# Performance work log

Measured on AMD Instinct MI355X. Metric: run time of the kernel, lower is better.

## Reference

```python
import jax, jax.numpy as jnp
import numpy as np

B, S, F, H = 512, 128, 128, 512
TIME_SCALE = 72.0
N_SUB = 8        # fixed RK45 substeps per interval (replaces adaptive dopri5 stepping)
MIN_DT = 1e-4    # torch code skips ODE solve if mean dt <= min_dt
LN_EPS = 1e-5


def setup_inputs() -> dict:
    key = jax.random.key(0)
    ks = jax.random.split(key, 12)
    time_points = jnp.sort(jax.random.uniform(ks[0], (B, S)) * TIME_SCALE, axis=1)
    values = jax.random.normal(ks[1], (B, S, F))
    s1 = 1.0 / np.sqrt(H)
    s2 = 1.0 / np.sqrt(2 * H)
    sg = 1.0 / np.sqrt(H)
    # ODEFunc: Linear(H,2H) -> tanh -> Linear(2H,H); weights stored (in,out)
    w1 = jax.random.uniform(ks[2], (H, 2 * H), minval=-s1, maxval=s1)
    b1 = jax.random.uniform(ks[3], (2 * H,), minval=-s1, maxval=s1)
    w2 = jax.random.uniform(ks[4], (2 * H, H), minval=-s2, maxval=s2)
    b2 = jax.random.uniform(ks[5], (H,), minval=-s2, maxval=s2)
    # GRUCell(F+1, H): torch layout w_ih (3H, F+1), w_hh (3H, H)
    w_ih = jax.random.uniform(ks[6], (3 * H, F + 1), minval=-sg, maxval=sg)
    w_hh = jax.random.uniform(ks[7], (3 * H, H), minval=-sg, maxval=sg)
    b_ih = jax.random.uniform(ks[8], (3 * H,), minval=-sg, maxval=sg)
    b_hh = jax.random.uniform(ks[9], (3 * H,), minval=-sg, maxval=sg)
    gamma = jnp.ones((H,))
    beta = jnp.zeros((H,))
    return {"time_points": time_points, "values": values,
            "w1": w1, "b1": b1, "w2": w2, "b2": b2,
            "w_ih": w_ih, "w_hh": w_hh, "b_ih": b_ih, "b_hh": b_hh,
            "gamma": gamma, "beta": beta}


def reference(time_points, values, w1, b1, w2, b2, w_ih, w_hh, b_ih, b_hh, gamma, beta):
    def ode_f(h):  # autonomous dynamics: 2-layer tanh MLP
        return jnp.tanh(h @ w1 + b1) @ w2 + b2

    def rk45(h, dt):  # Dormand-Prince 5th-order step (fixed step of size dt)
        k1 = ode_f(h)
        k2 = ode_f(h + dt * (1.0 / 5.0) * k1)
        k3 = ode_f(h + dt * (3.0 / 40.0 * k1 + 9.0 / 40.0 * k2))
        k4 = ode_f(h + dt * (44.0 / 45.0 * k1 - 56.0 / 15.0 * k2 + 32.0 / 9.0 * k3))
        k5 = ode_f(h + dt * (19372.0 / 6561.0 * k1 - 25360.0 / 2187.0 * k2
                             + 64448.0 / 6561.0 * k3 - 212.0 / 729.0 * k4))
        k6 = ode_f(h + dt * (9017.0 / 3168.0 * k1 - 355.0 / 33.0 * k2
                             + 46732.0 / 5247.0 * k3 + 49.0 / 176.0 * k4
                             - 5103.0 / 18656.0 * k5))
        return h + dt * (35.0 / 384.0 * k1 + 500.0 / 1113.0 * k3 + 125.0 / 192.0 * k4
                         - 2187.0 / 6784.0 * k5 + 11.0 / 84.0 * k6)

    batch, seq, _ = values.shape
    hdim = w_hh.shape[1]
    t_scaled_mean = (time_points / TIME_SCALE).mean(axis=0)  # (S,)
    dt_mean = jnp.concatenate([jnp.zeros((1,)), jnp.diff(t_scaled_mean)])  # (S,)
    dt_raw = jnp.concatenate([jnp.zeros((batch, 1)), jnp.diff(time_points, axis=1)], axis=1)  # (B,S)

    def step(h, inp):
        x, dti, dtm = inp  # x:(B,F), dti:(B,1), dtm: scalar
        dt_eff = jnp.where(dtm > MIN_DT, dtm, 0.0)
        sub = dt_eff / N_SUB
        h = jax.lax.fori_loop(0, N_SUB, lambda i, hh: rk45(hh, sub), h)
        x_aug = jnp.concatenate([x, dti], axis=-1)  # (B, F+1)
        gi = x_aug @ w_ih.T + b_ih
        gh = h @ w_hh.T + b_hh
        r = jax.nn.sigmoid(gi[:, :hdim] + gh[:, :hdim])
        z = jax.nn.sigmoid(gi[:, hdim:2 * hdim] + gh[:, hdim:2 * hdim])
        n = jnp.tanh(gi[:, 2 * hdim:] + r * gh[:, 2 * hdim:])
        h_new = (1.0 - z) * n + z * h
        return h_new, h_new

    h0 = jnp.zeros((batch, hdim), dtype=values.dtype)
    xs = (values.transpose(1, 0, 2), dt_raw.T[..., None], dt_mean)
    _, hs = jax.lax.scan(step, h0, xs)  # (S,B,H)
    rnn_out = hs.transpose(1, 0, 2)  # (B,S,H)
    mu = rnn_out.mean(axis=-1, keepdims=True)
    var = rnn_out.var(axis=-1, keepdims=True)
    return (rnn_out - mu) / jnp.sqrt(var + LN_EPS) * gamma + beta
```

## Files before the change

kernel.cpp:

```cpp
#include <hip/hip_runtime.h>
#include <cstdint>
#include <cstddef>

#define Bsz 512
#define Ssz 128
#define Fsz 128
#define Hsz 512
#define NTWO 1024

typedef __attribute__((ext_vector_type(8))) short short8;
typedef __attribute__((ext_vector_type(4))) float f32x4;
typedef unsigned int u32;
typedef unsigned short u16;

__device__ __forceinline__ float b2f(u16 u){
  union { u32 i; float f; } v; v.i = ((u32)u) << 16; return v.f;
}
__device__ __forceinline__ u16 f2b(float f){
  union { float f; u32 i; } v; v.f = f;
  u32 x = v.i;
  return (u16)((x + 0x7fffu + ((x >> 16) & 1u)) >> 16);
}
template<int AUX>
__device__ __forceinline__ void g2l16(const void* g, void* l){
  __builtin_amdgcn_global_load_lds((const __attribute__((address_space(1))) u32*)g,
                                   (__attribute__((address_space(3))) u32*)l, 16, 0, AUX);
}
__device__ __forceinline__ void st_devf(float* p, float v){
  __hip_atomic_store(p, v, __ATOMIC_RELAXED, __HIP_MEMORY_SCOPE_AGENT);
}
__device__ __forceinline__ void stg16_sc(void* p, short8 v){
  asm volatile("global_store_dwordx4 %0, %1, off sc0 sc1" :: "v"(p), "v"(v) : "memory");
}
__device__ __forceinline__ short8 ldg16(const void* p){
  short8 r;
  asm volatile("global_load_dwordx4 %0, %1, off" : "=v"(r) : "v"(p) : "memory");
  return r;
}
__device__ __forceinline__ float ftanh(float x){
  float a = fabsf(x);
  float e = __expf(-2.f*a);
  float t = __fdividef(1.f - e, 1.f + e);
  return copysignf(t, x);
}
__device__ __forceinline__ void vwait(int n){
  switch(n){
    case 0: asm volatile("s_waitcnt vmcnt(0)" ::: "memory"); break;
    case 1: asm volatile("s_waitcnt vmcnt(1)" ::: "memory"); break;
    case 2: asm volatile("s_waitcnt vmcnt(2)" ::: "memory"); break;
    case 4: asm volatile("s_waitcnt vmcnt(4)" ::: "memory"); break;
    default: break;
  }
}

#define RB1 0.09114583333333333f
#define RB3 0.4492362982929021f
#define RB4 0.6510416666666666f
#define RB5 (-0.3223921568627451f)
#define RB6 0.13095238095238096f
#define MFMA16 __builtin_amdgcn_mfma_f32_16x16x32_bf16


__global__ void zero_k(float* h, u16* h2, u32* bar){
  int i = blockIdx.x*256 + threadIdx.x;
  if (i < Bsz*Hsz) h[i] = 0.f;
  h2[i] = 0;
  if (i < 512) bar[i] = 0u;
}

__global__ void tsm_k(const float* tp, float* tsm){
  int s = blockIdx.x, tid = threadIdx.x;
  __shared__ float red[8];
  float v = tp[(size_t)tid*Ssz + s] + tp[(size_t)(tid + 256)*Ssz + s];
  int wave = tid >> 6, lane = tid & 63;
  for (int o = 32; o; o >>= 1) v += __shfl_down(v, o);
  if (!lane) red[wave] = v;
  __syncthreads();
  if (!tid) tsm[s] = (red[0] + red[1] + red[2] + red[3]) * (1.f/(512.f*72.f));
}

__global__ void sub_k(const float* tsm, float* subs){
  int i = threadIdx.x;
  if (i < Ssz){
    float dtm = (i == 0) ? 0.f : (tsm[i] - tsm[i-1]);
    float de = (dtm > 1e-4f) ? dtm : 0.f;
    subs[i] = de * 0.125f;
  }
}

__global__ void dti_k(const float* tp, float* dti){
  int i = blockIdx.x*256 + threadIdx.x;
  int ss = i & 127;
  dti[i] = ss ? (tp[i] - tp[i-1]) : 0.f;
}

__global__ void tr1_k(const float* w1, u16* lin, u16* swz){
  int i = blockIdx.x*256 + threadIdx.x;
  int n = i >> 9, k = i & 511;
  u16 v = f2b(w1[(size_t)k*NTWO + n]);
  lin[i] = v;
  swz[(size_t)n*512 + (k ^ ((n&7)<<3))] = v;
}

__global__ void cvt_k(const float* src, u16* dst, int n){
  int i = blockIdx.x*256 + threadIdx.x;
  if (i < n) dst[i] = f2b(src[i]);
}

__global__ void w2t_k(const float* w2, u16* dst){
  int i = blockIdx.x*256 + threadIdx.x;
  int n = i >> 10, k = i & 1023;
  dst[(size_t)n*1024 + (k ^ ((n&7)<<3))] = f2b(w2[(size_t)k*Hsz + n]);
}

__global__ void whh_k(const float* whh, u16* dst){
  int i = blockIdx.x*256 + threadIdx.x;
  int n = i >> 9, k = i & 511;
  dst[(size_t)n*512 + (k ^ ((n&7)<<3))] = f2b(whh[i]);
}

__global__ void wixs_k(const float* wih, u16* dst){
  int i = blockIdx.x*256 + threadIdx.x;
  int n = i >> 7, k = i & 127;
  dst[(size_t)n*128 + (k ^ ((n&7)<<3))] = f2b(wih[(size_t)n*129 + k]);
}

__global__ void wdt_k(const float* wih, float* wdt){
  int i = blockIdx.x*256 + threadIdx.x;
  if (i < 1536) wdt[i] = wih[(size_t)i*129 + 128];
}

__global__ void xsl_k(const float* vals, u16* dst){
  int i = blockIdx.x*256 + threadIdx.x;
  int p = i & 127;
  int b = (i >> 7) & 511;
  int s = i >> 16;
  int f = p ^ ((b&7)<<3);
  dst[i] = f2b(vals[((size_t)b*Ssz + s)*Fsz + f]);
}

__global__ void u_k(const float* b2v, const u16* w1t, float* u){
  int i = blockIdx.x*256 + threadIdx.x;
  if (i < NTWO){
    float acc = 0.f;
    for (int j = 0; j < Hsz; ++j) acc += b2v[j] * b2f(w1t[(size_t)i*Hsz + j]);
    u[i] = acc;
  }
}

struct GArgs {
  const u16* A; const u16* Bt;
  int a_rs, b_rs, K, kmask;
  u16* GtOut;
};

__launch_bounds__(256)
__global__ void gemm_k(GArgs g){
  __shared__ __align__(16) u16 lA[2][64*64];
  __shared__ __align__(16) u16 lB[2][32*64];
  const int tid = threadIdx.x;
  const int wave = tid >> 6, lane = tid & 63;
  const int quad = lane >> 4, l16 = lane & 15;
  const int mb = blockIdx.x * 64;
  const int nb = blockIdx.y * 32;
  f32x4 acc0 = {0.f,0.f,0.f,0.f}, acc1 = {0.f,0.f,0.f,0.f};

  const int r0 = tid >> 3,         c0 = (tid & 7) ^ (r0 & 7);
  const int r1 = (256 + tid) >> 3, c1 = (tid & 7) ^ (r1 & 7);

  const int am = wave*16 + l16;
  const int aoff0 = am*64 + (((quad    ) ^ (am & 7)) << 3);
  const int aoff1 = am*64 + (((4 + quad) ^ (am & 7)) << 3);
  const int bn0 = l16, bn1 = 16 + l16;
  const int boff00 = bn0*64 + (((quad    ) ^ (bn0 & 7)) << 3);
  const int boff01 = bn0*64 + (((4 + quad) ^ (bn0 & 7)) << 3);
  const int boff10 = bn1*64 + (((quad    ) ^ (bn1 & 7)) << 3);
  const int boff11 = bn1*64 + (((4 + quad) ^ (bn1 & 7)) << 3);

  const int nkb = g.K >> 6;
  {
    g2l16<0>(g.A  + (size_t)(mb + r0) * g.a_rs + ((c0 << 3)),             &lA[0][tid << 3]);
    g2l16<0>(g.A  + (size_t)(mb + r1) * g.a_rs + ((c1 << 3)),             &lA[0][(256 + tid) << 3]);
    g2l16<0>(g.Bt + (size_t)(nb + r0) * g.b_rs + (((c0 << 3)) & g.kmask), &lB[0][tid << 3]);
  }
  __syncthreads();
  for (int kb = 0; kb < nkb; ++kb){
    int buf = kb & 1;
    if (kb + 1 < nkb){
      int k0 = (kb + 1) << 6, nbuf = buf ^ 1;
      g2l16<0>(g.A  + (size_t)(mb + r0) * g.a_rs + (k0 + (c0 << 3)),             &lA[nbuf][tid << 3]);
      g2l16<0>(g.A  + (size_t)(mb + r1) * g.a_rs + (k0 + (c1 << 3)),             &lA[nbuf][(256 + tid) << 3]);
      g2l16<0>(g.Bt + (size_t)(nb + r0) * g.b_rs + ((k0 + (c0 << 3)) & g.kmask), &lB[nbuf][tid << 3]);
    }
    short8 a0  = *(const short8*)&lA[buf][aoff0];
    short8 a1  = *(const short8*)&lA[buf][aoff1];
    short8 b00 = *(const short8*)&lB[buf][boff00];
    short8 b01 = *(const short8*)&lB[buf][boff01];
    short8 b10 = *(const short8*)&lB[buf][boff10];
    short8 b11 = *(const short8*)&lB[buf][boff11];
    acc0 = MFMA16(a0, b00, acc0, 0, 0, 0);
    acc0 = MFMA16(a1, b01, acc0, 0, 0, 0);
    acc1 = MFMA16(a0, b10, acc1, 0, 0, 0);
    acc1 = MFMA16(a1, b11, acc1, 0, 0, 0);
    __syncthreads();
  }
  #pragma unroll
  for (int cb = 0; cb < 2; ++cb){
    f32x4 a = cb ? acc1 : acc0;
    int n = nb + cb*16 + l16;
    #pragma unroll
    for (int r = 0; r < 4; ++r){
      int m = mb + wave*16 + quad*4 + r;
      g.GtOut[(size_t)m*NTWO + n] = f2b(a[r]);
    }
  }
}


struct FArgs {
  const u16 *Gt, *w1t, *w2t, *whh, *wix, *xs;
  u16 *t, *Ta, *h2;
  float *h, *GI, *GH, *out;
  const float *subs, *dti, *u, *b1, *b2, *bhh, *bih, *wdt, *gamma, *beta;
  u32 *bar;
};

__launch_bounds__(512, 2)
__global__ void fused_k(FArgs f){
  __shared__ __align__(16) u16 sAfull[16*1024];
  __shared__ __align__(16) u16 sBring[3][8192];
  __shared__ __align__(16) u16 sTpack[2][2048];
  __shared__ float sRed[1024];
  __shared__ float sLN[16];

  const int tid = threadIdx.x;
  const int wave = tid >> 6, lane = tid & 63;
  const int quad = (lane >> 4) & 3, l16 = lane & 15;
  const int l7 = l16 & 7;
  const int bid = blockIdx.x;
  const int g   = bid & 31;
  const int jb  = bid >> 5;
  const int r0  = g * 16;
  const int cb0 = jb * 128;
  const int wcol = wave*16 + l16;
  const int cw4 = (wave & 3)*16 + l16;

  u32* flagp = f.bar + g*16;
  u32 epA = 1, epW = 0;
  u16* sBflat = &sBring[0][0];

  const int   pcol = cb0 + wcol;
  const float uuv = f.u[pcol], bb1v = f.b1[pcol];
  const int   fcol = jb*64 + cw4;
  const float b2v = f.b2[fcol];
  const int   gcol1 = jb*192 + wcol;
  const int   gcol2 = jb*192 + 128 + cw4;
  const float bhh1 = f.bhh[gcol1], bih1 = f.bih[gcol1], wdt1 = f.wdt[gcol1];
  const float bhh2 = f.bhh[gcol2], bih2 = f.bih[gcol2], wdt2 = f.wdt[gcol2];
  const int   b0row = r0 + jb*2;
  const int   j0 = tid & 255, grow = tid >> 8;
  const float gmA = f.gamma[j0], gmB = f.gamma[j0+256];
  const float btA = f.beta[j0],  btB = f.beta[j0+256];
  const size_t TSZ = (size_t)Bsz*NTWO;

  if (tid == 0)
    __hip_atomic_store(&flagp[jb], 1u, __ATOMIC_RELAXED, __HIP_MEMORY_SCOPE_AGENT);

  auto arrive = [&](){
    ++epA;
    if (tid == 0)
      __hip_atomic_store(&flagp[jb], epA, __ATOMIC_RELAXED, __HIP_MEMORY_SCOPE_AGENT);
  };
  auto waitall = [&](){
    ++epW;
    if (wave == 0){
      for (;;){
        u32 fv = (lane < 8)
          ? __hip_atomic_load(&flagp[lane], __ATOMIC_RELAXED, __HIP_MEMORY_SCOPE_AGENT)
          : 0xFFFFFFFFu;
        if (__all(fv >= epW)) break;
        __builtin_amdgcn_s_sleep(1);
      }
    }
    __syncthreads();
  };

  auto stageA16 = [&](const u16* gsrc){
    #pragma unroll
    for (int i = 0; i < 4; ++i){
      int u = tid + i*512; int row = u >> 7; int k8 = u & 127;
      g2l16<16>(gsrc + (((size_t)(r0+row)) << 10) + (k8 << 3), &sAfull[u << 3]);
    }
  };
  auto stageB2 = [&](const u16* gB, int burow, int bc, int slot){
    #pragma unroll
    for (int i = 0; i < 2; ++i){
      int u = tid + i*512; int col = u >> 3; int k8 = u & 7;
      g2l16<0>(gB + (size_t)col*(burow<<3) + (bc<<6) + (k8<<3), &sBring[slot][u << 3]);
    }
  };
  auto stageB1 = [&](const u16* gB, int burow, int bc, int slot){
    int col = tid >> 3; int k8 = tid & 7;
    g2l16<0>(gB + (size_t)col*(burow<<3) + (bc<<6) + (k8<<3), &sBring[slot][tid << 3]);
  };
  auto afrag = [&](int c, int kk)->short8 {
    return *(const short8*)&sAfull[(l16<<10) + (((c*8 + kk*4 + quad) ^ l7)<<3)];
  };
  auto bfragW = [&](int slot, int kk)->short8 {
    return *(const short8*)&sBring[slot][(wcol<<6) + ((((kk<<2)+quad) ^ (wcol&7))<<3)];
  };
  auto bfrag4 = [&](int slot, int kk)->short8 {
    return *(const short8*)&sBring[slot][(cw4<<6) + ((((kk<<2)+quad) ^ (cw4&7))<<3)];
  };

  f32x4 p_, T_, q0, q1, q2, q3, q4;
  short8 bfr[32];

  for (int s = 0; s < Ssz; ++s){
    const float sub = f.subs[s];
    const bool act = (sub > 0.f);

    waitall();

    if (act){
      {
        stageA16(f.h2);
        const u16* wb = f.w1t + ((size_t)cb0)*512;
        stageB2(wb, 64, 0, 0); stageB2(wb, 64, 1, 1);
        f32x4 acc = {0.f,0.f,0.f,0.f};
        for (int c = 0; c < 16; ++c){
          vwait((c+1 < 16) ? 2 : 0);
          __builtin_amdgcn_s_barrier();
          if (c+2 < 16) stageB2(wb, 64, (c+2)&7, (c+2)%3);
          short8 a0 = afrag(c,0), a1 = afrag(c,1);
          short8 b0 = bfragW(c%3,0), b1 = bfragW(c%3,1);
          acc = MFMA16(a0, b0, acc, 0,0,0);
          acc = MFMA16(a1, b1, acc, 0,0,0);
        }
        __syncthreads();
        #pragma unroll
        for (int r = 0; r < 4; ++r){
          float v = acc[r] + bb1v; p_[r] = v;
          float tv = ftanh(v);     T_[r] = sub*RB1*tv;
          sTpack[0][(quad*4+r)*128 + wcol] = f2b(tv);
        }
        __syncthreads();
        if (tid < 256){
          int row = tid >> 4, c8 = tid & 15;
          short8 v = *(const short8*)&sTpack[0][tid << 3];
          stg16_sc(f.t + (((size_t)(r0+row))<<10) + ((size_t)((jb<<4) + (c8 ^ (row&7)))<<3), v);
        }
        vwait(0); __syncthreads();
        arrive();
      }

      {
        const u16* gtb = f.Gt + ((size_t)pcol << 10) + (quad << 3);
        #pragma unroll
        for (int cc = 0; cc < 32; ++cc) bfr[cc] = ldg16(gtb + cc*32);
        vwait(0);
      }

      int par = 0;
      for (int ssb = 0; ssb < 8; ++ssb){
        for (int st = 1; st <= 6; ++st){
          if (ssb == 7 && st == 6) break;
          const int wt = (ssb == 7 && st == 5) ? 1 : 0;
          waitall();
          stageA16(f.t + (size_t)par*TSZ);
          vwait(0); __syncthreads();
          f32x4 aA = {0.f,0.f,0.f,0.f}, aB = {0.f,0.f,0.f,0.f};
          #pragma unroll
          for (int cc = 0; cc < 32; cc += 2){
            short8 x0 = *(const short8*)&sAfull[(l16<<10) + ((((cc<<2)+quad) ^ l7)<<3)];
            short8 x1 = *(const short8*)&sAfull[(l16<<10) + (((((cc+1)<<2)+quad) ^ l7)<<3)];
            aA = MFMA16(x0, bfr[cc],   aA, 0,0,0);
            aB = MFMA16(x1, bfr[cc+1], aB, 0,0,0);
          }
          f32x4 acc; 
          #pragma unroll
          for (int r = 0; r < 4; ++r) acc[r] = aA[r] + aB[r];
          #pragma unroll
          for (int r = 0; r < 4; ++r){
            float qv = acc[r] + uuv;
            float zs;
            if (st == 1){ q0[r] = qv; zs = 0.2f*qv; }
            else if (st == 2){ q1[r] = qv; zs = 0.075f*q0[r] + 0.225f*qv; }
            else if (st == 3){ q2[r] = qv;
              zs = (44.f/45.f)*q0[r] + (-56.f/15.f)*q1[r] + (32.f/9.f)*qv; }
            else if (st == 4){ q3[r] = qv;
              zs = 2.9525986892242035f*q0[r] + (-11.595793324188385f)*q1[r]
                 + 9.822892851699436f*q2[r] + (-0.2908093278463649f)*qv; }
            else if (st == 5){ q4[r] = qv;
              zs = 2.8462752525252526f*q0[r] + (-10.757575757575758f)*q1[r]
                 + 8.906422717743473f*q2[r] + 0.2784090909090909f*q3[r]
                 + (-0.2735313036020583f)*qv; }
            else {
              zs = RB1*q0[r] + RB3*q2[r] + RB4*q3[r] + RB5*q4[r] + RB6*qv;
            }
            float tv;
            if (st < 6){
              float z = p_[r] + sub*zs;
              tv = ftanh(z);
              if (st >= 2){
                float bn = (st == 2) ? RB3 : (st == 3) ? RB4 : (st == 4) ? RB5 : RB6;
                T_[r] += sub*bn*tv;
              }
            } else {
              p_[r] += sub*zs;
              tv = ftanh(p_[r]);
              T_[r] += sub*RB1*tv;
            }
            sTpack[0][(quad*4+r)*128 + wcol] = f2b(wt ? T_[r] : tv);
          }
          __syncthreads();
          if (tid < 256){
            int row = tid >> 4, c8 = tid & 15;
            short8 v = *(const short8*)&sTpack[0][tid << 3];
            u16* dst = wt ? f.Ta : (f.t + (size_t)(par^1)*TSZ);
            stg16_sc(dst + (((size_t)(r0+row))<<10) + ((size_t)((jb<<4) + (c8 ^ (row&7)))<<3), v);
          }
          vwait(0); __syncthreads();
          arrive();
          par ^= 1;
        }
      }

      {
        waitall();
        stageA16(f.Ta);
        const u16* wb = f.w2t + ((size_t)(jb*64)) * 1024;
        stageB1(wb, 128, 0, 0); stageB1(wb, 128, 1, 1);
        f32x4 fa = {0.f,0.f,0.f,0.f};
        for (int c = 0; c < 16; ++c){
          vwait((c+1 < 16) ? 1 : 0);
          __builtin_amdgcn_s_barrier();
          if (c+2 < 16) stageB1(wb, 128, c+2, (c+2)%3);
          if ((c >> 3) == (wave >> 2)){
            short8 a0 = afrag(c,0), a1 = afrag(c,1);
            short8 b0 = bfrag4(c%3,0), b1 = bfrag4(c%3,1);
            fa = MFMA16(a0, b0, fa, 0,0,0);
            fa = MFMA16(a1, b1, fa, 0,0,0);
          }
        }
        __syncthreads();
        if (tid < 256){
          int row = tid >> 4, c4 = tid & 15;
          g2l16<16>(f.h + (size_t)(r0+row)*512 + jb*64 + (c4<<2), &sBflat[tid << 3]);
        }
        if (wave >= 4){
          #pragma unroll
          for (int r = 0; r < 4; ++r)
            sRed[(wave&3)*256 + (quad*4+r)*16 + l16] = fa[r];
        }
        __syncthreads();
        if (wave < 4){
          vwait(0);
          const float* HS = (const float*)sBflat;
          #pragma unroll
          for (int r = 0; r < 4; ++r){
            int lrow = quad*4 + r;
            float hv = HS[lrow*64 + cw4] + fa[r] + sRed[(wave&3)*256 + lrow*16 + l16]
                     + 8.f*sub*b2v;
            st_devf(&f.h[(size_t)(r0+lrow)*512 + fcol], hv);
            u16 hi = f2b(hv);
            sTpack[0][lrow*64 + cw4] = hi;
            sTpack[0][1024 + lrow*64 + cw4] = f2b(hv - b2f(hi));
          }
        }
        __syncthreads();
        if (tid < 256){
          int half = tid >> 7, row = (tid >> 3) & 15, c8 = tid & 7;
          short8 v = *(const short8*)&sTpack[0][tid << 3];
          size_t gu = (((size_t)(r0+row)) << 7) + (half<<6) + (jb<<3) + (c8 ^ (row&7));
          stg16_sc(f.h2 + (gu << 3), v);
        }
        vwait(0); __syncthreads();
        arrive();
        waitall();
      }
    }

    {
      stageA16(f.h2);
      const u16* wb1 = f.whh + ((size_t)(jb*192)) * 512;
      stageB2(wb1, 64, 0, 0); stageB2(wb1, 64, 1, 1);
      f32x4 gh = {0.f,0.f,0.f,0.f};
      for (int c = 0; c < 16; ++c){
        vwait((c+1 < 16) ? 2 : 0);
        __builtin_amdgcn_s_barrier();
        if (c+2 < 16) stageB2(wb1, 64, (c+2)&7, (c+2)%3);
        short8 a0 = afrag(c,0), a1 = afrag(c,1);
        short8 b0 = bfragW(c%3,0), b1 = bfragW(c%3,1);
        gh = MFMA16(a0, b0, gh, 0,0,0);
        gh = MFMA16(a1, b1, gh, 0,0,0);
      }
      #pragma unroll
      for (int r = 0; r < 4; ++r)
        st_devf(&f.GH[(size_t)(r0+quad*4+r)*1536 + gcol1], gh[r] + bhh1);
      __syncthreads();
      const u16* wb2 = f.whh + ((size_t)(jb*192+128)) * 512;
      stageB1(wb2, 64, 0, 0); stageB1(wb2, 64, 1, 1);
      f32x4 g2 = {0.f,0.f,0.f,0.f};
      for (int c = 0; c < 8; ++c){
        vwait((c+1 < 8) ? 1 : 0);
        __builtin_amdgcn_s_barrier();
        if (c+2 < 8) stageB1(wb2, 64, c+2, (c+2)%3);
        int ac = c + ((wave >= 4) ? 8 : 0);
        short8 a0 = afrag(ac,0), a1 = afrag(ac,1);
        short8 b0 = bfrag4(c%3,0), b1 = bfrag4(c%3,1);
        g2 = MFMA16(a0, b0, g2, 0,0,0);
        g2 = MFMA16(a1, b1, g2, 0,0,0);
      }
      __syncthreads();
      if (wave >= 4){
        #pragma unroll
        for (int r = 0; r < 4; ++r)
          sRed[(wave&3)*256 + (quad*4+r)*16 + l16] = g2[r];
      }
      __syncthreads();
      if (wave < 4){
        #pragma unroll
        for (int r = 0; r < 4; ++r){
          float v = g2[r] + sRed[wave*256 + (quad*4+r)*16 + l16];
          st_devf(&f.GH[(size_t)(r0+quad*4+r)*1536 + gcol2], v + bhh2);
        }
      }
      __syncthreads();
    }

    {
      if (tid < 256){
        int row = tid >> 4, k16 = tid & 15;
        g2l16<0>(f.xs + (((size_t)s*512 + r0 + row) << 7) + (k16 << 3), &sAfull[tid << 3]);
      }
      #pragma unroll
      for (int i = 0; i < 6; ++i){
        int u = tid + i*512; int col = u >> 4; int k16 = u & 15;
        g2l16<0>(f.wix + (((size_t)(jb*192 + col)) << 7) + (k16 << 3), &sBflat[u << 3]);
      }
      vwait(0); __syncthreads();
      f32x4 gi = {0.f,0.f,0.f,0.f};
      #pragma unroll
      for (int c = 0; c < 4; ++c){
        short8 a = *(const short8*)&sAfull[(l16<<7) + ((((c<<2)+quad) ^ l7)<<3)];
        short8 b = *(const short8*)&sBflat[(wcol<<7) + ((((c<<2)+quad) ^ (wcol&7))<<3)];
        gi = MFMA16(a, b, gi, 0,0,0);
      }
      #pragma unroll
      for (int r = 0; r < 4; ++r){
        float dv = f.dti[((size_t)(r0+quad*4+r) << 7) + s];
        st_devf(&f.GI[(size_t)(r0+quad*4+r)*1536 + gcol1], gi[r] + bih1 + dv*wdt1);
      }
      if (wave < 4){
        int cw2 = 128 + cw4;
        f32x4 gi2 = {0.f,0.f,0.f,0.f};
        #pragma unroll
        for (int c = 0; c < 4; ++c){
          short8 a = *(const short8*)&sAfull[(l16<<7) + ((((c<<2)+quad) ^ l7)<<3)];
          short8 b = *(const short8*)&sBflat[(cw2<<7) + ((((c<<2)+quad) ^ (cw2&7))<<3)];
          gi2 = MFMA16(a, b, gi2, 0,0,0);
        }
        #pragma unroll
        for (int r = 0; r < 4; ++r){
          float dv = f.dti[((size_t)(r0+quad*4+r) << 7) + s];
          st_devf(&f.GI[(size_t)(r0+quad*4+r)*1536 + gcol2], gi2[r] + bih2 + dv*wdt2);
        }
      }
      vwait(0); __syncthreads();
      arrive();
    }

    {
      waitall();
      #pragma unroll
      for (int i = 0; i < 4; ++i){
        int u = tid + i*512;
        if (u < 1792){
          const float* src;
          if (u < 768){ int row = (u >= 384); int off = u - row*384;
            src = f.GI + (size_t)(b0row+row)*1536 + (off<<2); }
          else if (u < 1536){ int v2 = u - 768; int row = (v2 >= 384); int off = v2 - row*384;
            src = f.GH + (size_t)(b0row+row)*1536 + (off<<2); }
          else { int v2 = u - 1536; int row = v2 >> 7; int off = v2 & 127;
            src = f.h + (size_t)(b0row+row)*512 + (off<<2); }
          g2l16<16>(src, &sAfull[u << 3]);
        }
      }
      vwait(0); __syncthreads();
      const float* LSf = (const float*)sAfull;
      const float* GIr = LSf + grow*1536;
      const float* GHr = LSf + 3072 + grow*1536;
      const float* Hr  = LSf + 6144 + grow*512;
      float hn0, hn1;
      {
        float gr = GIr[j0] + GHr[j0];
        float gz = GIr[512 + j0] + GHr[512 + j0];
        float ng = ftanh(GIr[1024 + j0] + (1.f/(1.f + __expf(-gr)))*GHr[1024 + j0]);
        float zg = 1.f/(1.f + __expf(-gz));
        hn0 = (1.f - zg)*ng + zg*Hr[j0];
      }
      {
        int j = j0 + 256;
        float gr = GIr[j] + GHr[j];
        float gz = GIr[512 + j] + GHr[512 + j];
        float ng = ftanh(GIr[1024 + j] + (1.f/(1.f + __expf(-gr)))*GHr[1024 + j]);
        float zg = 1.f/(1.f + __expf(-gz));
        hn1 = (1.f - zg)*ng + zg*Hr[j];
      }
      st_devf(&f.h[(size_t)(b0row+grow)*512 + j0], hn0);
      st_devf(&f.h[(size_t)(b0row+grow)*512 + j0 + 256], hn1);
      u16* sT = &sTpack[0][0];
      u16 hi0 = f2b(hn0);
      sT[grow*1024 + j0]       = hi0;
      sT[grow*1024 + 512 + j0] = f2b(hn0 - b2f(hi0));
      u16 hi1 = f2b(hn1);
      sT[grow*1024 + 256 + j0] = hi1;
      sT[grow*1024 + 768 + j0] = f2b(hn1 - b2f(hi1));
      float sm = hn0 + hn1;
      for (int o = 32; o; o >>= 1) sm += __shfl_down(sm, o);
      if (!lane) sLN[wave] = sm;
      __syncthreads();
      if (tid == 0 || tid == 256){
        int rr = tid >> 8;
        sLN[8+rr] = (sLN[rr*4]+sLN[rr*4+1]+sLN[rr*4+2]+sLN[rr*4+3]) * (1.f/512.f);
      }
      __syncthreads();
      float mu = sLN[8+grow];
      float d0 = hn0 - mu, d1 = hn1 - mu;
      float ss = d0*d0 + d1*d1;
      for (int o = 32; o; o >>= 1) ss += __shfl_down(ss, o);
      if (!lane) sLN[wave] = ss;
      __syncthreads();
      if (tid == 0 || tid == 256){
        int rr = tid >> 8;
        sLN[12+rr] = rsqrtf((sLN[rr*4]+sLN[rr*4+1]+sLN[rr*4+2]+sLN[rr*4+3]) * (1.f/512.f) + 1e-5f);
      }
      __syncthreads();
      float isd = sLN[12+grow];
      size_t ob = ((size_t)(b0row+grow)*128 + s)*512;
      f.out[ob + j0]       = d0*isd*gmA + btA;
      f.out[ob + j0 + 256] = d1*isd*gmB + btB;
      __syncthreads();
      if (tid < 256){
        int row = tid >> 7, u8 = tid & 127;
        int b = b0row + row;
        short8 v = *(const short8*)&sT[(row*128 + u8) << 3];
        stg16_sc(f.h2 + (((size_t)b) << 10) + ((size_t)(u8 ^ (b&7)) << 3), v);
      }
      vwait(0); __syncthreads();
      arrive();
    }
  }
}


extern "C" void kernel_launch(void* const* d_in, const int* in_sizes, int n_in,
                              void* d_out, int out_size, void* d_ws, size_t ws_size,
                              hipStream_t stream){
  (void)in_sizes; (void)n_in; (void)out_size; (void)ws_size;
  const float* tp    = (const float*)d_in[0];
  const float* vals  = (const float*)d_in[1];
  const float* w1    = (const float*)d_in[2];
  const float* b1v   = (const float*)d_in[3];
  const float* w2    = (const float*)d_in[4];
  const float* b2v   = (const float*)d_in[5];
  const float* wih   = (const float*)d_in[6];
  const float* whh   = (const float*)d_in[7];
  const float* bih   = (const float*)d_in[8];
  const float* bhh   = (const float*)d_in[9];
  const float* gamma = (const float*)d_in[10];
  const float* beta  = (const float*)d_in[11];
  float* out = (float*)d_out;

  uint8_t* w = (uint8_t*)d_ws;
  size_t off = 0;
  auto alloc = [&](size_t bytes)->void*{
    void* pp = w + off; off += (bytes + 255) & ~(size_t)255; return pp; };
  float* h      = (float*)alloc((size_t)Bsz*Hsz*4);
  u16*   h2     = (u16*)alloc((size_t)Bsz*NTWO*2);
  u16*   tbuf   = (u16*)alloc((size_t)2*Bsz*NTWO*2);
  u16*   Ta     = (u16*)alloc((size_t)Bsz*NTWO*2);
  float* GH     = (float*)alloc((size_t)Bsz*1536*4);
  float* GI     = (float*)alloc((size_t)Bsz*1536*4);
  u16*   Gt     = (u16*)alloc((size_t)NTWO*NTWO*2);
  u16*   w1tl   = (u16*)alloc((size_t)NTWO*Hsz*2);
  u16*   w1ts   = (u16*)alloc((size_t)NTWO*Hsz*2);
  u16*   w2bf   = (u16*)alloc((size_t)NTWO*Hsz*2);
  u16*   w2ts   = (u16*)alloc((size_t)Hsz*NTWO*2);
  u16*   whhs   = (u16*)alloc((size_t)1536*Hsz*2);
  u16*   wixs   = (u16*)alloc((size_t)1536*128*2);
  u16*   xs     = (u16*)alloc((size_t)Ssz*Bsz*Fsz*2);
  float* wdt    = (float*)alloc(1536*4);
  float* uvec   = (float*)alloc(NTWO*4);
  float* tsm    = (float*)alloc(Ssz*4);
  float* subs   = (float*)alloc(Ssz*4);
  float* dti    = (float*)alloc((size_t)Bsz*Ssz*4);
  u32*   bar    = (u32*)alloc(2048);

  hipLaunchKernelGGL(zero_k, dim3(2048), dim3(256), 0, stream, h, h2, bar);
  hipLaunchKernelGGL(tsm_k,  dim3(128),  dim3(256), 0, stream, tp, tsm);
  hipLaunchKernelGGL(sub_k,  dim3(1),    dim3(128), 0, stream, tsm, subs);
  hipLaunchKernelGGL(dti_k,  dim3(256),  dim3(256), 0, stream, tp, dti);
  hipLaunchKernelGGL(tr1_k,  dim3(2048), dim3(256), 0, stream, w1, w1tl, w1ts);
  hipLaunchKernelGGL(cvt_k,  dim3(2048), dim3(256), 0, stream, w2, w2bf, NTWO*Hsz);
  hipLaunchKernelGGL(w2t_k,  dim3(2048), dim3(256), 0, stream, w2, w2ts);
  hipLaunchKernelGGL(whh_k,  dim3(3072), dim3(256), 0, stream, whh, whhs);
  hipLaunchKernelGGL(wixs_k, dim3(768),  dim3(256), 0, stream, wih, wixs);
  hipLaunchKernelGGL(wdt_k,  dim3(6),    dim3(256), 0, stream, wih, wdt);
  hipLaunchKernelGGL(xsl_k,  dim3(32768),dim3(256), 0, stream, vals, xs);
  hipLaunchKernelGGL(u_k,    dim3(4),    dim3(256), 0, stream, b2v, w1tl, uvec);
  {
    GArgs g{};
    g.A = w1tl; g.Bt = w2bf; g.a_rs = Hsz; g.b_rs = Hsz; g.K = Hsz;
    g.kmask = 511; g.GtOut = Gt;
    hipLaunchKernelGGL(gemm_k, dim3(16,32), dim3(256), 0, stream, g);
  }

  FArgs fa{};
  fa.Gt = Gt; fa.w1t = w1ts; fa.w2t = w2ts; fa.whh = whhs; fa.wix = wixs; fa.xs = xs;
  fa.t = tbuf; fa.Ta = Ta; fa.h2 = h2;
  fa.h = h; fa.GI = GI; fa.GH = GH; fa.out = out;
  fa.subs = subs; fa.dti = dti; fa.u = uvec; fa.b1 = b1v; fa.b2 = b2v;
  fa.bhh = bhh; fa.bih = bih; fa.wdt = wdt; fa.gamma = gamma; fa.beta = beta;
  fa.bar = bar;

  void* params[] = { (void*)&fa };
  hipError_t e = hipLaunchCooperativeKernel((const void*)fused_k, dim3(256), dim3(512),
                                            params, 0u, stream);
  if (e != hipSuccess){
    hipLaunchKernelGGL(fused_k, dim3(256), dim3(512), 0, stream, fa);
  }
}
```

Measured before the change: 31.42 ms.

## Detect XCD co-location at runtime and pipeline ODE-stage A loads in chunks

At kernel start each block records which XCD it runs on (via s_getreg) and the blocks compare these IDs. If all eight blocks of a group share one XCD, the body is instantiated with a cache-policy bit (AUX=1) for the cross-block loads in place of the previous AUX=16. In either mode, the ODE-stage A operand is now staged in four chunks with partial vmcnt waits, so MFMAs start before the whole tile has arrived. The startup adds an all-blocks spin handshake. Coherence of the shared h/t buffers now depends on the XCD-mapping check being correct.

```diff
diff --git a/kernel.cpp b/kernel.cpp
--- a/kernel.cpp
+++ b/kernel.cpp
@@ -48,6 +48,7 @@
     case 0: asm volatile("s_waitcnt vmcnt(0)" ::: "memory"); break;
     case 1: asm volatile("s_waitcnt vmcnt(1)" ::: "memory"); break;
     case 2: asm volatile("s_waitcnt vmcnt(2)" ::: "memory"); break;
+    case 3: asm volatile("s_waitcnt vmcnt(3)" ::: "memory"); break;
     case 4: asm volatile("s_waitcnt vmcnt(4)" ::: "memory"); break;
     default: break;
   }
@@ -65,7 +66,7 @@
   int i = blockIdx.x*256 + threadIdx.x;
   if (i < Bsz*Hsz) h[i] = 0.f;
   h2[i] = 0;
-  if (i < 512) bar[i] = 0u;
+  if (i < 2304) bar[i] = 0u;
 }
 
 __global__ void tsm_k(const float* tp, float* tsm){
@@ -225,19 +226,20 @@
   u32 *bar;
 };
 
-__launch_bounds__(512, 2)
-__global__ void fused_k(FArgs f){
-  __shared__ __align__(16) u16 sAfull[16*1024];
-  __shared__ __align__(16) u16 sBring[3][8192];
-  __shared__ __align__(16) u16 sTpack[2][2048];
-  __shared__ float sRed[1024];
-  __shared__ float sLN[16];
-
-  const int tid = threadIdx.x;
+struct Sh {
+  __align__(16) u16 sAfull[16*1024];
+  __align__(16) u16 sBring[3][8192];
+  __align__(16) u16 sTpack[2][2048];
+  __align__(16) float sRed[1024];
+  float sLN[16];
+  int mode;
+};
+
+template<int AUXD>
+__device__ __forceinline__ void run_body(const FArgs& f, Sh& S, const int tid, const int bid){
   const int wave = tid >> 6, lane = tid & 63;
   const int quad = (lane >> 4) & 3, l16 = lane & 15;
   const int l7 = l16 & 7;
-  const int bid = blockIdx.x;
   const int g   = bid & 31;
   const int jb  = bid >> 5;
   const int r0  = g * 16;
@@ -247,7 +249,7 @@
 
   u32* flagp = f.bar + g*16;
   u32 epA = 1, epW = 0;
-  u16* sBflat = &sBring[0][0];
+  u16* sBflat = &S.sBring[0][0];
 
   const int   pcol = cb0 + wcol;
   const float uuv = f.u[pcol], bb1v = f.b1[pcol];
@@ -289,32 +291,55 @@
     #pragma unroll
     for (int i = 0; i < 4; ++i){
       int u = tid + i*512; int row = u >> 7; int k8 = u & 127;
-      g2l16<16>(gsrc + (((size_t)(r0+row)) << 10) + (k8 << 3), &sAfull[u << 3]);
+      g2l16<AUXD>(gsrc + (((size_t)(r0+row)) << 10) + (k8 << 3), &S.sAfull[u << 3]);
     }
   };
   auto stageB2 = [&](const u16* gB, int burow, int bc, int slot){
     #pragma unroll
     for (int i = 0; i < 2; ++i){
       int u = tid + i*512; int col = u >> 3; int k8 = u & 7;
-      g2l16<0>(gB + (size_t)col*(burow<<3) + (bc<<6) + (k8<<3), &sBring[slot][u << 3]);
+      g2l16<0>(gB + (size_t)col*(burow<<3) + (bc<<6) + (k8<<3), &S.sBring[slot][u << 3]);
     }
   };
   auto stageB1 = [&](const u16* gB, int burow, int bc, int slot){
     int col = tid >> 3; int k8 = tid & 7;
-    g2l16<0>(gB + (size_t)col*(burow<<3) + (bc<<6) + (k8<<3), &sBring[slot][tid << 3]);
+    g2l16<0>(gB + (size_t)col*(burow<<3) + (bc<<6) + (k8<<3), &S.sBring[slot][tid << 3]);
   };
   auto afrag = [&](int c, int kk)->short8 {
-    return *(const short8*)&sAfull[(l16<<10) + (((c*8 + kk*4 + quad) ^ l7)<<3)];
+    return *(const short8*)&S.sAfull[(l16<<10) + (((c*8 + kk*4 + quad) ^ l7)<<3)];
   };
   auto bfragW = [&](int slot, int kk)->short8 {
-    return *(const short8*)&sBring[slot][(wcol<<6) + ((((kk<<2)+quad) ^ (wcol&7))<<3)];
+    return *(const short8*)&S.sBring[slot][(wcol<<6) + ((((kk<<2)+quad) ^ (wcol&7))<<3)];
   };
   auto bfrag4 = [&](int slot, int kk)->short8 {
-    return *(const short8*)&sBring[slot][(cw4<<6) + ((((kk<<2)+quad) ^ (cw4&7))<<3)];
+    return *(const short8*)&S.sBring[slot][(cw4<<6) + ((((kk<<2)+quad) ^ (cw4&7))<<3)];
   };
 
   f32x4 p_, T_, q0, q1, q2, q3, q4;
   short8 bfr[32];
+
+  auto ode_stage = [&](const u16* tb, f32x4& aA, f32x4& aB){
+    #pragma unroll
+    for (int i = 0; i < 4; ++i){
+      int c = i*4 + (tid>>7);
+      int uu = tid & 127;
+      int row = uu >> 3, k8o = uu & 7;
+      g2l16<AUXD>(tb + (((size_t)(r0+row))<<10) + ((size_t)((c<<3)+k8o)<<3),
+                  &S.sAfull[(c<<10) + (uu<<3)]);
+    }
+    #pragma unroll
+    for (int ci = 0; ci < 4; ++ci){
+      vwait(3-ci);
+      __builtin_amdgcn_s_barrier();
+      #pragma unroll
+      for (int cc = ci*4; cc < ci*4+4; ++cc){
+        short8 x0 = *(const short8*)&S.sAfull[(cc<<10) + (l16<<6) + (((quad    ) ^ l7)<<3)];
+        short8 x1 = *(const short8*)&S.sAfull[(cc<<10) + (l16<<6) + (((4 + quad) ^ l7)<<3)];
+        aA = MFMA16(x0, bfr[2*cc],   aA, 0,0,0);
+        aB = MFMA16(x1, bfr[2*cc+1], aB, 0,0,0);
+      }
+    }
+  };
 
   for (int s = 0; s < Ssz; ++s){
     const float sub = f.subs[s];
@@ -342,12 +367,12 @@
         for (int r = 0; r < 4; ++r){
           float v = acc[r] + bb1v; p_[r] = v;
           float tv = ftanh(v);     T_[r] = sub*RB1*tv;
-          sTpack[0][(quad*4+r)*128 + wcol] = f2b(tv);
+          S.sTpack[0][(quad*4+r)*128 + wcol] = f2b(tv);
         }
         __syncthreads();
         if (tid < 256){
           int row = tid >> 4, c8 = tid & 15;
-          short8 v = *(const short8*)&sTpack[0][tid << 3];
+          short8 v = *(const short8*)&S.sTpack[0][tid << 3];
           stg16_sc(f.t + (((size_t)(r0+row))<<10) + ((size_t)((jb<<4) + (c8 ^ (row&7)))<<3), v);
         }
         vwait(0); __syncthreads();
@@ -367,22 +392,11 @@
           if (ssb == 7 && st == 6) break;
           const int wt = (ssb == 7 && st == 5) ? 1 : 0;
           waitall();
-          stageA16(f.t + (size_t)par*TSZ);
-          vwait(0); __syncthreads();
           f32x4 aA = {0.f,0.f,0.f,0.f}, aB = {0.f,0.f,0.f,0.f};
-          #pragma unroll
-          for (int cc = 0; cc < 32; cc += 2){
-            short8 x0 = *(const short8*)&sAfull[(l16<<10) + ((((cc<<2)+quad) ^ l7)<<3)];
-            short8 x1 = *(const short8*)&sAfull[(l16<<10) + (((((cc+1)<<2)+quad) ^ l7)<<3)];
-            aA = MFMA16(x0, bfr[cc],   aA, 0,0,0);
-            aB = MFMA16(x1, bfr[cc+1], aB, 0,0,0);
-          }
-          f32x4 acc; 
-          #pragma unroll
-          for (int r = 0; r < 4; ++r) acc[r] = aA[r] + aB[r];
+          ode_stage(f.t + (size_t)par*TSZ, aA, aB);
           #pragma unroll
           for (int r = 0; r < 4; ++r){
-            float qv = acc[r] + uuv;
+            float qv = aA[r] + aB[r] + uuv;
             float zs;
             if (st == 1){ q0[r] = qv; zs = 0.2f*qv; }
             else if (st == 2){ q1[r] = qv; zs = 0.075f*q0[r] + 0.225f*qv; }
@@ -411,12 +425,12 @@
               tv = ftanh(p_[r]);
               T_[r] += sub*RB1*tv;
             }
-            sTpack[0][(quad*4+r)*128 + wcol] = f2b(wt ? T_[r] : tv);
+            S.sTpack[0][(quad*4+r)*128 + wcol] = f2b(wt ? T_[r] : tv);
           }
           __syncthreads();
           if (tid < 256){
             int row = tid >> 4, c8 = tid & 15;
-            short8 v = *(const short8*)&sTpack[0][tid << 3];
+            short8 v = *(const short8*)&S.sTpack[0][tid << 3];
             u16* dst = wt ? f.Ta : (f.t + (size_t)(par^1)*TSZ);
             stg16_sc(dst + (((size_t)(r0+row))<<10) + ((size_t)((jb<<4) + (c8 ^ (row&7)))<<3), v);
           }
@@ -446,12 +460,12 @@
         __syncthreads();
         if (tid < 256){
           int row = tid >> 4, c4 = tid & 15;
-          g2l16<16>(f.h + (size_t)(r0+row)*512 + jb*64 + (c4<<2), &sBflat[tid << 3]);
+          g2l16<AUXD>(f.h + (size_t)(r0+row)*512 + jb*64 + (c4<<2), &sBflat[tid << 3]);
         }
         if (wave >= 4){
           #pragma unroll
           for (int r = 0; r < 4; ++r)
-            sRed[(wave&3)*256 + (quad*4+r)*16 + l16] = fa[r];
+            S.sRed[(wave&3)*256 + (quad*4+r)*16 + l16] = fa[r];
         }
         __syncthreads();
         if (wave < 4){
@@ -460,18 +474,18 @@
           #pragma unroll
           for (int r = 0; r < 4; ++r){
             int lrow = quad*4 + r;
-            float hv = HS[lrow*64 + cw4] + fa[r] + sRed[(wave&3)*256 + lrow*16 + l16]
+            float hv = HS[lrow*64 + cw4] + fa[r] + S.sRed[(wave&3)*256 + lrow*16 + l16]
                      + 8.f*sub*b2v;
             st_devf(&f.h[(size_t)(r0+lrow)*512 + fcol], hv);
             u16 hi = f2b(hv);
-            sTpack[0][lrow*64 + cw4] = hi;
-            sTpack[0][1024 + lrow*64 + cw4] = f2b(hv - b2f(hi));
+            S.sTpack[0][lrow*64 + cw4] = hi;
+            S.sTpack[0][1024 + lrow*64 + cw4] = f2b(hv - b2f(hi));
           }
         }
         __syncthreads();
         if (tid < 256){
           int half = tid >> 7, row = (tid >> 3) & 15, c8 = tid & 7;
-          short8 v = *(const short8*)&sTpack[0][tid << 3];
+          short8 v = *(const short8*)&S.sTpack[0][tid << 3];
           size_t gu = (((size_t)(r0+row)) << 7) + (half<<6) + (jb<<3) + (c8 ^ (row&7));
           stg16_sc(f.h2 + (gu << 3), v);
         }
@@ -516,13 +530,13 @@
       if (wave >= 4){
         #pragma unroll
         for (int r = 0; r < 4; ++r)
-          sRed[(wave&3)*256 + (quad*4+r)*16 + l16] = g2[r];
+          S.sRed[(wave&3)*256 + (quad*4+r)*16 + l16] = g2[r];
       }
       __syncthreads();
       if (wave < 4){
         #pragma unroll
         for (int r = 0; r < 4; ++r){
-          float v = g2[r] + sRed[wave*256 + (quad*4+r)*16 + l16];
+          float v = g2[r] + S.sRed[wave*256 + (quad*4+r)*16 + l16];
           st_devf(&f.GH[(size_t)(r0+quad*4+r)*1536 + gcol2], v + bhh2);
         }
       }
@@ -532,7 +546,7 @@
     {
       if (tid < 256){
         int row = tid >> 4, k16 = tid & 15;
-        g2l16<0>(f.xs + (((size_t)s*512 + r0 + row) << 7) + (k16 << 3), &sAfull[tid << 3]);
+        g2l16<0>(f.xs + (((size_t)s*512 + r0 + row) << 7) + (k16 << 3), &S.sAfull[tid << 3]);
       }
       #pragma unroll
       for (int i = 0; i < 6; ++i){
@@ -543,7 +557,7 @@
       f32x4 gi = {0.f,0.f,0.f,0.f};
       #pragma unroll
       for (int c = 0; c < 4; ++c){
-        short8 a = *(const short8*)&sAfull[(l16<<7) + ((((c<<2)+quad) ^ l7)<<3)];
+        short8 a = *(const short8*)&S.sAfull[(l16<<7) + ((((c<<2)+quad) ^ l7)<<3)];
         short8 b = *(const short8*)&sBflat[(wcol<<7) + ((((c<<2)+quad) ^ (wcol&7))<<3)];
         gi = MFMA16(a, b, gi, 0,0,0);
       }
@@ -557,7 +571,7 @@
         f32x4 gi2 = {0.f,0.f,0.f,0.f};
         #pragma unroll
         for (int c = 0; c < 4; ++c){
-          short8 a = *(const short8*)&sAfull[(l16<<7) + ((((c<<2)+quad) ^ l7)<<3)];
+          short8 a = *(const short8*)&S.sAfull[(l16<<7) + ((((c<<2)+quad) ^ l7)<<3)];
           short8 b = *(const short8*)&sBflat[(cw2<<7) + ((((c<<2)+quad) ^ (cw2&7))<<3)];
           gi2 = MFMA16(a, b, gi2, 0,0,0);
         }
@@ -584,11 +598,11 @@
             src = f.GH + (size_t)(b0row+row)*1536 + (off<<2); }
           else { int v2 = u - 1536; int row = v2 >> 7; int off = v2 & 127;
             src = f.h + (size_t)(b0row+row)*512 + (off<<2); }
-          g2l16<16>(src, &sAfull[u << 3]);
+          g2l16<AUXD>(src, &S.sAfull[u << 3]);
         }
       }
       vwait(0); __syncthreads();
-      const float* LSf = (const float*)sAfull;
+      const float* LSf = (const float*)S.sAfull;
       const float* GIr = LSf + grow*1536;
       const float* GHr = LSf + 3072 + grow*1536;
       const float* Hr  = LSf + 6144 + grow*512;
@@ -610,7 +624,7 @@
       }
       st_devf(&f.h[(size_t)(b0row+grow)*512 + j0], hn0);
       st_devf(&f.h[(size_t)(b0row+grow)*512 + j0 + 256], hn1);
-      u16* sT = &sTpack[0][0];
+      u16* sT = &S.sTpack[0][0];
       u16 hi0 = f2b(hn0);
       sT[grow*1024 + j0]       = hi0;
       sT[grow*1024 + 512 + j0] = f2b(hn0 - b2f(hi0));
@@ -619,25 +633,25 @@
       sT[grow*1024 + 768 + j0] = f2b(hn1 - b2f(hi1));
       float sm = hn0 + hn1;
       for (int o = 32; o; o >>= 1) sm += __shfl_down(sm, o);
-      if (!lane) sLN[wave] = sm;
+      if (!lane) S.sLN[wave] = sm;
       __syncthreads();
       if (tid == 0 || tid == 256){
         int rr = tid >> 8;
-        sLN[8+rr] = (sLN[rr*4]+sLN[rr*4+1]+sLN[rr*4+2]+sLN[rr*4+3]) * (1.f/512.f);
-      }
-      __syncthreads();
-      float mu = sLN[8+grow];
+        S.sLN[8+rr] = (S.sLN[rr*4]+S.sLN[rr*4+1]+S.sLN[rr*4+2]+S.sLN[rr*4+3]) * (1.f/512.f);
+      }
+      __syncthreads();
+      float mu = S.sLN[8+grow];
       float d0 = hn0 - mu, d1 = hn1 - mu;
       float ss = d0*d0 + d1*d1;
       for (int o = 32; o; o >>= 1) ss += __shfl_down(ss, o);
-      if (!lane) sLN[wave] = ss;
+      if (!lane) S.sLN[wave] = ss;
       __syncthreads();
       if (tid == 0 || tid == 256){
         int rr = tid >> 8;
-        sLN[12+rr] = rsqrtf((sLN[rr*4]+sLN[rr*4+1]+sLN[rr*4+2]+sLN[rr*4+3]) * (1.f/512.f) + 1e-5f);
-      }
-      __syncthreads();
-      float isd = sLN[12+grow];
+        S.sLN[12+rr] = rsqrtf((S.sLN[rr*4]+S.sLN[rr*4+1]+S.sLN[rr*4+2]+S.sLN[rr*4+3]) * (1.f/512.f) + 1e-5f);
+      }
+      __syncthreads();
+      float isd = S.sLN[12+grow];
       size_t ob = ((size_t)(b0row+grow)*128 + s)*512;
       f.out[ob + j0]       = d0*isd*gmA + btA;
       f.out[ob + j0 + 256] = d1*isd*gmB + btB;
@@ -652,6 +666,41 @@
       arrive();
     }
   }
+}
+
+__launch_bounds__(512, 2)
+__global__ void fused_k(FArgs f){
+  __shared__ Sh S;
+  const int tid = threadIdx.x, bid = blockIdx.x;
+  const int g = bid & 31;
+  {
+    u32* xa = f.bar + 2048;
+    if (tid == 0){
+      u32 xcc = ((u32)__builtin_amdgcn_s_getreg(63508) & 0xFu) + 1u;
+      __hip_atomic_store(&xa[bid], xcc, __ATOMIC_RELAXED, __HIP_MEMORY_SCOPE_AGENT);
+    }
+    if (tid < 256){
+      u32 v;
+      do {
+        v = __hip_atomic_load(&xa[tid], __ATOMIC_RELAXED, __HIP_MEMORY_SCOPE_AGENT);
+        if (!v) __builtin_amdgcn_s_sleep(4);
+      } while (!v);
+      ((u32*)S.sRed)[tid] = v;
+    }
+    __syncthreads();
+    if (tid == 0){
+      const u32* xv = (const u32*)S.sRed;
+      u32 v0 = xv[g];
+      int eq = 1;
+      for (int j = 1; j < 8; ++j) eq &= (xv[g + 32*j] == v0);
+      int cnt = 0;
+      for (int i = 0; i < 256; ++i) cnt += (xv[i] == v0);
+      S.mode = (eq && cnt == 32) ? 1 : 0;
+    }
+    __syncthreads();
+  }
+  if (S.mode) run_body<1>(f, S, tid, bid);
+  else        run_body<16>(f, S, tid, bid);
 }
 
 
@@ -696,7 +745,7 @@
   float* tsm    = (float*)alloc(Ssz*4);
   float* subs   = (float*)alloc(Ssz*4);
   float* dti    = (float*)alloc((size_t)Bsz*Ssz*4);
-  u32*   bar    = (u32*)alloc(2048);
+  u32*   bar    = (u32*)alloc(16384);
 
   hipLaunchKernelGGL(zero_k, dim3(2048), dim3(256), 0, stream, h, h2, bar);
   hipLaunchKernelGGL(tsm_k,  dim3(128),  dim3(256), 0, stream, tp, tsm);
```

After: 30.25 ms. 3.7% less time.
